# Kernel optimization log

Hardware: AMD Instinct MI355X
Metric: run time of the kernel (lower is better)

Reference implementation:

```python
import jax, jax.numpy as jnp
import numpy as np

N_NODES = 100000


def _sage_conv(x, src, dst, W_l, b_l, W_r, num_nodes):
    # PyG SAGEConv (aggr='mean'): out = lin_l(mean_j x_j) + lin_r(x)
    msg = x[src]                                                   # [E, d] gather
    s = jax.ops.segment_sum(msg, dst, num_segments=num_nodes)      # [N, d]
    cnt = jax.ops.segment_sum(jnp.ones((src.shape[0], 1), x.dtype), dst,
                              num_segments=num_nodes)              # [N, 1]
    agg = s / jnp.maximum(cnt, 1)                                  # mean, 0 if no neighbors
    return agg @ W_l.T + b_l + x @ W_r.T


def setup_inputs() -> dict:
    key = jax.random.key(0)
    ks = jax.random.split(key, 8)
    d = 64
    E = 1600000
    scale = 1.0 / np.sqrt(d)
    x = jax.random.normal(ks[0], (N_NODES, d), dtype=jnp.float32)
    edge_index = jax.random.randint(ks[1], (2, E), 0, N_NODES, dtype=jnp.int64)
    W1_l = jax.random.normal(ks[2], (d, d), dtype=jnp.float32) * scale
    b1_l = jnp.zeros((d,), dtype=jnp.float32)
    W1_r = jax.random.normal(ks[3], (d, d), dtype=jnp.float32) * scale
    W2_l = jax.random.normal(ks[4], (d, d), dtype=jnp.float32) * scale
    b2_l = jnp.zeros((d,), dtype=jnp.float32)
    W2_r = jax.random.normal(ks[5], (d, d), dtype=jnp.float32) * scale
    return {"x": x, "edge_index": edge_index, "W1_l": W1_l, "b1_l": b1_l,
            "W1_r": W1_r, "W2_l": W2_l, "b2_l": b2_l, "W2_r": W2_r}


def reference(x, edge_index, W1_l, b1_l, W1_r, W2_l, b2_l, W2_r):
    src, dst = edge_index[0], edge_index[1]
    h = jax.nn.relu(_sage_conv(x, src, dst, W1_l, b1_l, W1_r, N_NODES))
    h = jax.nn.relu(_sage_conv(h, src, dst, W2_l, b2_l, W2_r, N_NODES))
    return h
```

## Files before the change

### kernel.cpp

```cpp
#include <hip/hip_runtime.h>
#include <hip/hip_fp16.h>


#define NFEAT 64
#define NPB 128
#define NBUCK 782
#define MAXPB 2560
#define TILE 4096

typedef _Float16 h8 __attribute__((ext_vector_type(8)));
typedef _Float16 h4 __attribute__((ext_vector_type(4)));
typedef float f4 __attribute__((ext_vector_type(4)));

__global__ __launch_bounds__(512) void bscatter_k(const int* __restrict__ src,
                                                  const int* __restrict__ dst,
                                                  int* __restrict__ gcur,
                                                  int* __restrict__ pairs, int E) {
  __shared__ int lcnt[NBUCK];
  __shared__ int loff[NBUCK];
  __shared__ int lcur[NBUCK];
  __shared__ int lbase[NBUCK];
  __shared__ int s_packed[TILE];
  __shared__ unsigned short s_b[TILE];

  int tid = threadIdx.x;
  int tileStart = blockIdx.x * TILE;
  int tileCnt = E - tileStart; if (tileCnt > TILE) tileCnt = TILE;

  for (int t = tid; t < NBUCK; t += 512) lcnt[t] = 0;
  __syncthreads();

  int ep[8], eb[8];
  int base = tileStart + tid * 8;
  int ne = 0;
  if (base + 7 < E) {
    int4 a0 = *(const int4*)(src + base);
    int4 a1 = *(const int4*)(src + base + 4);
    int4 b0 = *(const int4*)(dst + base);
    int4 b1 = *(const int4*)(dst + base + 4);
    int es[8] = {a0.x,a0.y,a0.z,a0.w,a1.x,a1.y,a1.z,a1.w};
    int ed[8] = {b0.x,b0.y,b0.z,b0.w,b1.x,b1.y,b1.z,b1.w};
#pragma unroll
    for (int j = 0; j < 8; ++j) {
      eb[j] = ed[j] >> 7;
      ep[j] = es[j] | ((ed[j] & 127) << 17);
    }
    ne = 8;
  } else {
    for (int j = 0; j < 8 && base + j < E; ++j) {
      int s = src[base + j], d = dst[base + j];
      eb[j] = d >> 7;
      ep[j] = s | ((d & 127) << 17);
      ++ne;
    }
  }
  for (int j = 0; j < ne; ++j) atomicAdd(&lcnt[eb[j]], 1);
  __syncthreads();

  if (tid < 64) {
    int carry = 0;
    for (int cb = 0; cb < NBUCK; cb += 64) {
      int i = cb + tid;
      int v = (i < NBUCK) ? lcnt[i] : 0;
      int x = v;
#pragma unroll
      for (int d = 1; d < 64; d <<= 1) {
        int y = __shfl_up(x, d);
        if (tid >= d) x += y;
      }
      if (i < NBUCK) { int e = x - v + carry; loff[i] = e; lcur[i] = e; }
      carry += __shfl(x, 63);
    }
  }
  __syncthreads();

  for (int t = tid; t < NBUCK; t += 512) {
    int v = lcnt[t];
    if (v) lbase[t] = atomicAdd(&gcur[t], v);
  }
  __syncthreads();

  for (int j = 0; j < ne; ++j) {
    int b = eb[j];
    int slot = atomicAdd(&lcur[b], 1);
    s_packed[slot] = ep[j];
    s_b[slot] = (unsigned short)b;
  }
  __syncthreads();

  for (int k = tid; k < tileCnt; k += 512) {
    int b = s_b[k];
    int g = lbase[b] + (k - loff[b]);
    if (g < MAXPB) pairs[(size_t)b * MAXPB + g] = s_packed[k];
  }
}

__global__ __launch_bounds__(256) void regroup_k(const int* __restrict__ gcur,
                                                 const int* __restrict__ pairs,
                                                 int* __restrict__ csr,
                                                 int* __restrict__ off,
                                                 int* __restrict__ cnt,
                                                 float* __restrict__ inv, int n) {
  __shared__ int lcnt[NPB];
  __shared__ int lofs[NPB];
  __shared__ int lcur[NPB];
  __shared__ int stage[MAXPB];

  int tid = threadIdx.x;
  int b = blockIdx.x;
  int nbase = b << 7;
  int nn = n - nbase; if (nn > NPB) nn = NPB;
  if (nn <= 0) return;

  int m = gcur[b]; if (m > MAXPB) m = MAXPB;
  const int* seg = pairs + (size_t)b * MAXPB;

  if (tid < NPB) lcnt[tid] = 0;
  __syncthreads();

  for (int e = tid; e < m; e += 256)
    atomicAdd(&lcnt[(seg[e] >> 17) & 127], 1);
  __syncthreads();

  if (tid < 64) {
    int carry = 0;
#pragma unroll
    for (int cb = 0; cb < NPB; cb += 64) {
      int i = cb + tid;
      int v = lcnt[i];
      int x = v;
#pragma unroll
      for (int d = 1; d < 64; d <<= 1) {
        int y = __shfl_up(x, d);
        if (tid >= d) x += y;
      }
      int e = x - v + carry;
      lofs[i] = e; lcur[i] = e;
      carry += __shfl(x, 63);
    }
  }
  __syncthreads();

  for (int e = tid; e < m; e += 256) {
    int p = seg[e];
    int slot = atomicAdd(&lcur[(p >> 17) & 127], 1);
    stage[slot] = p & 0x1FFFF;
  }
  __syncthreads();

  for (int k = tid; k < m; k += 256) csr[(size_t)b * MAXPB + k] = stage[k];
  for (int t = tid; t < nn; t += 256) {
    int c = lcnt[t];
    cnt[nbase + t] = c;
    off[nbase + t] = b * MAXPB + lofs[t];
    inv[nbase + t] = 1.0f / (float)(c > 1 ? c : 1);
  }
}

__device__ inline h8 cvt8(const float* p) {
  float4 lo = *(const float4*)p;
  float4 hi = *(const float4*)(p + 4);
  h8 f;
  f[0]=(_Float16)lo.x; f[1]=(_Float16)lo.y; f[2]=(_Float16)lo.z; f[3]=(_Float16)lo.w;
  f[4]=(_Float16)hi.x; f[5]=(_Float16)hi.y; f[6]=(_Float16)hi.z; f[7]=(_Float16)hi.w;
  return f;
}
__device__ inline h8 cvt8(const __half* p) { return *(const h8*)p; }

template <typename InT>
__global__ __launch_bounds__(256) void gemm_k(const InT* __restrict__ X,
                                              const float* __restrict__ Wl,
                                              const float* __restrict__ Wr,
                                              const float* __restrict__ bias,
                                              __half* __restrict__ Zh,
                                              __half* __restrict__ Ph, int n) {
  int tid = threadIdx.x;
  int wave = tid >> 6, lane = tid & 63;
  int m = lane & 15, quad = lane >> 4;
  int row0 = (blockIdx.x * 4 + wave) * 16;
  if (row0 >= n) return;

  h8 wf[2][4][2];
#pragma unroll
  for (int mat = 0; mat < 2; ++mat) {
    const float* W = mat ? Wr : Wl;
#pragma unroll
    for (int t = 0; t < 4; ++t)
#pragma unroll
      for (int s = 0; s < 2; ++s)
        wf[mat][t][s] = cvt8(W + (t * 16 + m) * 64 + s * 32 + quad * 8);
  }

  int rowm = row0 + m; if (rowm > n - 1) rowm = n - 1;
  const InT* xp = X + (size_t)rowm * 64 + quad * 8;
  h8 af0 = cvt8(xp);
  h8 af1 = cvt8(xp + 32);

  f4 accz[4], accp[4];
#pragma unroll
  for (int t = 0; t < 4; ++t) {
    f4 z; z[0]=0.f; z[1]=0.f; z[2]=0.f; z[3]=0.f;
    float4 bl = *(const float4*)(bias + t * 16 + quad * 4);
    f4 p; p[0]=bl.x; p[1]=bl.y; p[2]=bl.z; p[3]=bl.w;
    z = __builtin_amdgcn_mfma_f32_16x16x32_f16(wf[0][t][0], af0, z, 0, 0, 0);
    z = __builtin_amdgcn_mfma_f32_16x16x32_f16(wf[0][t][1], af1, z, 0, 0, 0);
    p = __builtin_amdgcn_mfma_f32_16x16x32_f16(wf[1][t][0], af0, p, 0, 0, 0);
    p = __builtin_amdgcn_mfma_f32_16x16x32_f16(wf[1][t][1], af1, p, 0, 0, 0);
    accz[t] = z;
    accp[t] = p;
  }

  if (row0 + m < n) {
    size_t base = (size_t)(row0 + m) * NFEAT + quad * 4;
#pragma unroll
    for (int t = 0; t < 4; ++t) {
      h4 zv, pv;
#pragma unroll
      for (int r = 0; r < 4; ++r) {
        zv[r] = (_Float16)accz[t][r];
        pv[r] = (_Float16)accp[t][r];
      }
      *(h4*)(Zh + base + t * 16) = zv;
      *(h4*)(Ph + base + t * 16) = pv;
    }
  }
}

__device__ inline float2 h2f(unsigned u) {
  __half2 h = *reinterpret_cast<__half2*>(&u);
  return __half22float2(h);
}

__device__ inline void store8(float* op, const float* r) {
  float4 r0, r1;
  r0.x=r[0]; r0.y=r[1]; r0.z=r[2]; r0.w=r[3];
  r1.x=r[4]; r1.y=r[5]; r1.z=r[6]; r1.w=r[7];
  *(float4*)(op) = r0;
  *(float4*)(op + 4) = r1;
}
__device__ inline void store8(__half* op, const float* r) {
  h8 v;
#pragma unroll
  for (int i = 0; i < 8; ++i) v[i] = (_Float16)r[i];
  *(h8*)op = v;
}

template <typename OutT>
__global__ __launch_bounds__(256) void agg_k(const int* __restrict__ off,
                                             const int* __restrict__ cnt,
                                             const float* __restrict__ inv,
                                             const int* __restrict__ csr,
                                             const __half* __restrict__ Z,
                                             const __half* __restrict__ Pin,
                                             OutT* __restrict__ out, int n) {
  int t = blockIdx.x * 256 + threadIdx.x;
  int node = t >> 3;
  if (node >= n) return;
  int q = t & 7;

  int start = off[node];
  int deg = cnt[node];

  float a[8];
#pragma unroll
  for (int i = 0; i < 8; ++i) a[i] = 0.f;
  for (int j = 0; j < deg; ++j) {
    int nb = csr[start + j];
    uint4 raw = *(const uint4*)(Z + (size_t)nb * NFEAT + q * 8);
    float2 f0 = h2f(raw.x), f1 = h2f(raw.y), f2 = h2f(raw.z), f3 = h2f(raw.w);
    a[0] += f0.x; a[1] += f0.y; a[2] += f1.x; a[3] += f1.y;
    a[4] += f2.x; a[5] += f2.y; a[6] += f3.x; a[7] += f3.y;
  }

  float iv = inv[node];
  uint4 praw = *(const uint4*)(Pin + (size_t)node * NFEAT + q * 8);
  float2 p0 = h2f(praw.x), p1 = h2f(praw.y), p2 = h2f(praw.z), p3 = h2f(praw.w);
  float r[8];
  r[0] = fmaxf(a[0] * iv + p0.x, 0.f);
  r[1] = fmaxf(a[1] * iv + p0.y, 0.f);
  r[2] = fmaxf(a[2] * iv + p1.x, 0.f);
  r[3] = fmaxf(a[3] * iv + p1.y, 0.f);
  r[4] = fmaxf(a[4] * iv + p2.x, 0.f);
  r[5] = fmaxf(a[5] * iv + p2.y, 0.f);
  r[6] = fmaxf(a[6] * iv + p3.x, 0.f);
  r[7] = fmaxf(a[7] * iv + p3.y, 0.f);
  store8(out + (size_t)node * NFEAT + q * 8, r);
}

extern "C" void kernel_launch(void* const* d_in, const int* in_sizes, int n_in,
                              void* d_out, int out_size, void* d_ws, size_t ws_size,
                              hipStream_t stream) {
  const float* x   = (const float*)d_in[0];
  const int*   ei  = (const int*)d_in[1];
  const float* W1l = (const float*)d_in[2];
  const float* b1  = (const float*)d_in[3];
  const float* W1r = (const float*)d_in[4];
  const float* W2l = (const float*)d_in[5];
  const float* b2  = (const float*)d_in[6];
  const float* W2r = (const float*)d_in[7];
  float* out = (float*)d_out;

  int N = in_sizes[0] / NFEAT;
  int E = in_sizes[1] / 2;
  const int* srcp = ei;
  const int* dstp = ei + E;

  char* w = (char*)d_ws;
  int*    pairs = (int*)w;    w += (size_t)NBUCK * MAXPB * 4;
  int*    csr   = (int*)w;    w += (size_t)NBUCK * MAXPB * 4;
  __half* Zh    = (__half*)w; w += (size_t)N * NFEAT * 2;
  __half* Ph    = (__half*)w; w += (size_t)N * NFEAT * 2;
  __half* H     = (__half*)w; w += (size_t)N * NFEAT * 2;
  int*    off   = (int*)w;    w += (size_t)N * 4;
  int*    cnt   = (int*)w;    w += (size_t)N * 4;
  float*  inv   = (float*)w;  w += (size_t)N * 4;
  int*    gcur  = (int*)w;    w += NBUCK * 4;
  if ((size_t)(w - (char*)d_ws) > ws_size) return;

  hipMemsetAsync(gcur, 0, NBUCK * 4, stream);

  int sb = (E + TILE - 1) / TILE;
  bscatter_k<<<sb, 512, 0, stream>>>(srcp, dstp, gcur, pairs, E);
  regroup_k<<<NBUCK, 256, 0, stream>>>(gcur, pairs, csr, off, cnt, inv, N);

  int gb = (N + 63) / 64;
  int ab = (N * 8 + 255) / 256;

  gemm_k<float><<<gb, 256, 0, stream>>>(x, W1l, W1r, b1, Zh, Ph, N);
  agg_k<__half><<<ab, 256, 0, stream>>>(off, cnt, inv, csr, Zh, Ph, H, N);
  gemm_k<__half><<<gb, 256, 0, stream>>>(H, W2l, W2r, b2, Zh, Ph, N);
  agg_k<float><<<ab, 256, 0, stream>>>(off, cnt, inv, csr, Zh, Ph, out, N);
}
```

Before: 267.7 us.

## Shrink scatter tiles, drop regroup LDS staging, process 32 rows per GEMM wave

The bucket-scatter kernel now uses 2048-edge tiles with 256 threads, which reduces LDS per block and launches more blocks. The regroup kernel keeps its loaded pairs in registers and writes CSR entries straight to global memory instead of staging them in a 2560-entry LDS array. This removes one barrier and the LDS footprint, but the global writes become scattered. The GEMM kernel handles two 16-row tiles per wave so each weight fragment load is reused, halving the grid size.

Measured after the change: 273.3 us. 2.1% more time.

```diff
diff --git a/kernel.cpp b/kernel.cpp
--- a/kernel.cpp
+++ b/kernel.cpp
@@ -6,13 +6,13 @@
 #define NPB 128
 #define NBUCK 782
 #define MAXPB 2560
-#define TILE 4096
+#define TILE 2048
 
 typedef _Float16 h8 __attribute__((ext_vector_type(8)));
 typedef _Float16 h4 __attribute__((ext_vector_type(4)));
 typedef float f4 __attribute__((ext_vector_type(4)));
 
-__global__ __launch_bounds__(512) void bscatter_k(const int* __restrict__ src,
+__global__ __launch_bounds__(256) void bscatter_k(const int* __restrict__ src,
                                                   const int* __restrict__ dst,
                                                   int* __restrict__ gcur,
                                                   int* __restrict__ pairs, int E) {
@@ -27,7 +27,7 @@
   int tileStart = blockIdx.x * TILE;
   int tileCnt = E - tileStart; if (tileCnt > TILE) tileCnt = TILE;
 
-  for (int t = tid; t < NBUCK; t += 512) lcnt[t] = 0;
+  for (int t = tid; t < NBUCK; t += 256) lcnt[t] = 0;
   __syncthreads();
 
   int ep[8], eb[8];
@@ -74,7 +74,7 @@
   }
   __syncthreads();
 
-  for (int t = tid; t < NBUCK; t += 512) {
+  for (int t = tid; t < NBUCK; t += 256) {
     int v = lcnt[t];
     if (v) lbase[t] = atomicAdd(&gcur[t], v);
   }
@@ -88,7 +88,7 @@
   }
   __syncthreads();
 
-  for (int k = tid; k < tileCnt; k += 512) {
+  for (int k = tid; k < tileCnt; k += 256) {
     int b = s_b[k];
     int g = lbase[b] + (k - loff[b]);
     if (g < MAXPB) pairs[(size_t)b * MAXPB + g] = s_packed[k];
@@ -104,7 +104,6 @@
   __shared__ int lcnt[NPB];
   __shared__ int lofs[NPB];
   __shared__ int lcur[NPB];
-  __shared__ int stage[MAXPB];
 
   int tid = threadIdx.x;
   int b = blockIdx.x;
@@ -118,8 +117,13 @@
   if (tid < NPB) lcnt[tid] = 0;
   __syncthreads();
 
-  for (int e = tid; e < m; e += 256)
-    atomicAdd(&lcnt[(seg[e] >> 17) & 127], 1);
+  int myv[(MAXPB + 255) / 256];
+  int mycnt = 0;
+  for (int e = tid; e < m; e += 256) {
+    int p = seg[e];
+    myv[mycnt++] = p;
+    atomicAdd(&lcnt[(p >> 17) & 127], 1);
+  }
   __syncthreads();
 
   if (tid < 64) {
@@ -141,14 +145,13 @@
   }
   __syncthreads();
 
-  for (int e = tid; e < m; e += 256) {
-    int p = seg[e];
+  int* csrseg = csr + (size_t)b * MAXPB;
+  for (int i = 0; i < mycnt; ++i) {
+    int p = myv[i];
     int slot = atomicAdd(&lcur[(p >> 17) & 127], 1);
-    stage[slot] = p & 0x1FFFF;
-  }
-  __syncthreads();
-
-  for (int k = tid; k < m; k += 256) csr[(size_t)b * MAXPB + k] = stage[k];
+    csrseg[slot] = p & 0x1FFFF;
+  }
+
   for (int t = tid; t < nn; t += 256) {
     int c = lcnt[t];
     cnt[nbase + t] = c;
@@ -177,51 +180,59 @@
   int tid = threadIdx.x;
   int wave = tid >> 6, lane = tid & 63;
   int m = lane & 15, quad = lane >> 4;
-  int row0 = (blockIdx.x * 4 + wave) * 16;
+  int row0 = (blockIdx.x * 4 + wave) * 32;
   if (row0 >= n) return;
 
-  h8 wf[2][4][2];
-#pragma unroll
-  for (int mat = 0; mat < 2; ++mat) {
-    const float* W = mat ? Wr : Wl;
-#pragma unroll
-    for (int t = 0; t < 4; ++t)
-#pragma unroll
-      for (int s = 0; s < 2; ++s)
-        wf[mat][t][s] = cvt8(W + (t * 16 + m) * 64 + s * 32 + quad * 8);
-  }
-
-  int rowm = row0 + m; if (rowm > n - 1) rowm = n - 1;
-  const InT* xp = X + (size_t)rowm * 64 + quad * 8;
-  h8 af0 = cvt8(xp);
-  h8 af1 = cvt8(xp + 32);
-
-  f4 accz[4], accp[4];
+  int rA = row0 + m;      if (rA > n - 1) rA = n - 1;
+  int rB = row0 + 16 + m; if (rB > n - 1) rB = n - 1;
+  const InT* xpA = X + (size_t)rA * 64 + quad * 8;
+  const InT* xpB = X + (size_t)rB * 64 + quad * 8;
+  h8 afA0 = cvt8(xpA), afA1 = cvt8(xpA + 32);
+  h8 afB0 = cvt8(xpB), afB1 = cvt8(xpB + 32);
+
+  f4 acczA[4], accpA[4], acczB[4], accpB[4];
 #pragma unroll
   for (int t = 0; t < 4; ++t) {
-    f4 z; z[0]=0.f; z[1]=0.f; z[2]=0.f; z[3]=0.f;
+    h8 wl0 = cvt8(Wl + (t * 16 + m) * 64 + quad * 8);
+    h8 wl1 = cvt8(Wl + (t * 16 + m) * 64 + 32 + quad * 8);
+    h8 wr0 = cvt8(Wr + (t * 16 + m) * 64 + quad * 8);
+    h8 wr1 = cvt8(Wr + (t * 16 + m) * 64 + 32 + quad * 8);
+
     float4 bl = *(const float4*)(bias + t * 16 + quad * 4);
-    f4 p; p[0]=bl.x; p[1]=bl.y; p[2]=bl.z; p[3]=bl.w;
-    z = __builtin_amdgcn_mfma_f32_16x16x32_f16(wf[0][t][0], af0, z, 0, 0, 0);
-    z = __builtin_amdgcn_mfma_f32_16x16x32_f16(wf[0][t][1], af1, z, 0, 0, 0);
-    p = __builtin_amdgcn_mfma_f32_16x16x32_f16(wf[1][t][0], af0, p, 0, 0, 0);
-    p = __builtin_amdgcn_mfma_f32_16x16x32_f16(wf[1][t][1], af1, p, 0, 0, 0);
-    accz[t] = z;
-    accp[t] = p;
-  }
-
-  if (row0 + m < n) {
-    size_t base = (size_t)(row0 + m) * NFEAT + quad * 4;
-#pragma unroll
-    for (int t = 0; t < 4; ++t) {
-      h4 zv, pv;
-#pragma unroll
-      for (int r = 0; r < 4; ++r) {
-        zv[r] = (_Float16)accz[t][r];
-        pv[r] = (_Float16)accp[t][r];
+    f4 z0; z0[0]=0.f; z0[1]=0.f; z0[2]=0.f; z0[3]=0.f;
+    f4 p0; p0[0]=bl.x; p0[1]=bl.y; p0[2]=bl.z; p0[3]=bl.w;
+    f4 z1 = z0, p1 = p0;
+
+    z0 = __builtin_amdgcn_mfma_f32_16x16x32_f16(wl0, afA0, z0, 0, 0, 0);
+    z0 = __builtin_amdgcn_mfma_f32_16x16x32_f16(wl1, afA1, z0, 0, 0, 0);
+    p0 = __builtin_amdgcn_mfma_f32_16x16x32_f16(wr0, afA0, p0, 0, 0, 0);
+    p0 = __builtin_amdgcn_mfma_f32_16x16x32_f16(wr1, afA1, p0, 0, 0, 0);
+    z1 = __builtin_amdgcn_mfma_f32_16x16x32_f16(wl0, afB0, z1, 0, 0, 0);
+    z1 = __builtin_amdgcn_mfma_f32_16x16x32_f16(wl1, afB1, z1, 0, 0, 0);
+    p1 = __builtin_amdgcn_mfma_f32_16x16x32_f16(wr0, afB0, p1, 0, 0, 0);
+    p1 = __builtin_amdgcn_mfma_f32_16x16x32_f16(wr1, afB1, p1, 0, 0, 0);
+    acczA[t] = z0; accpA[t] = p0;
+    acczB[t] = z1; accpB[t] = p1;
+  }
+
+#pragma unroll
+  for (int half = 0; half < 2; ++half) {
+    int r = row0 + half * 16 + m;
+    if (r < n) {
+      size_t base = (size_t)r * NFEAT + quad * 4;
+      f4* az = half ? acczB : acczA;
+      f4* ap = half ? accpB : accpA;
+#pragma unroll
+      for (int t = 0; t < 4; ++t) {
+        h4 zv, pv;
+#pragma unroll
+        for (int k = 0; k < 4; ++k) {
+          zv[k] = (_Float16)az[t][k];
+          pv[k] = (_Float16)ap[t][k];
+        }
+        *(h4*)(Zh + base + t * 16) = zv;
+        *(h4*)(Ph + base + t * 16) = pv;
       }
-      *(h4*)(Zh + base + t * 16) = zv;
-      *(h4*)(Ph + base + t * 16) = pv;
     }
   }
 }
@@ -320,10 +331,10 @@
   hipMemsetAsync(gcur, 0, NBUCK * 4, stream);
 
   int sb = (E + TILE - 1) / TILE;
-  bscatter_k<<<sb, 512, 0, stream>>>(srcp, dstp, gcur, pairs, E);
+  bscatter_k<<<sb, 256, 0, stream>>>(srcp, dstp, gcur, pairs, E);
   regroup_k<<<NBUCK, 256, 0, stream>>>(gcur, pairs, csr, off, cnt, inv, N);
 
-  int gb = (N + 63) / 64;
+  int gb = (N + 127) / 128;
   int ab = (N * 8 + 255) / 256;
 
   gemm_k<float><<<gb, 256, 0, stream>>>(x, W1l, W1r, b1, Zh, Ph, N);
```
